# Performance work log

Hardware: AMD Instinct MI355X
Metric: run time of the kernel (lower is better)

## Reference

```python
import jax, jax.numpy as jnp
import numpy as np

EPS = 1e-5  # torch LayerNorm default eps

def _mish(x):
    return x * jnp.tanh(jax.nn.softplus(x))

def _ln(x, g, b):
    mu = jnp.mean(x, axis=-1, keepdims=True)
    var = jnp.mean(jnp.square(x - mu), axis=-1, keepdims=True)
    return (x - mu) * jax.lax.rsqrt(var + EPS) * g + b

def setup_inputs() -> dict:
    key = jax.random.key(0)
    ks = jax.random.split(key, 10)
    B, D, O1, O2, O3 = 65536, 784, 512, 264, 128
    def lin(k, fan_in, shape):
        bound = 1.0 / np.sqrt(fan_in)
        return jax.random.uniform(k, shape, jnp.float32, -bound, bound)
    return {
        "x":  jax.random.uniform(ks[0], (B, D), jnp.float32),
        "W1": lin(ks[1], D,  (O1, D)),   # enFC1, bias=False
        "g1": jnp.ones((O1,), jnp.float32), "b1": jnp.zeros((O1,), jnp.float32),
        "W2": lin(ks[2], O1, (O2, O1)),  # enFC2, bias=False
        "g2": jnp.ones((O2,), jnp.float32), "b2": jnp.zeros((O2,), jnp.float32),
        "W3": lin(ks[3], O2, (O3, O2)),  # enFC3 with bias
        "b3": lin(ks[4], O2, (O3,)),
        "gh": jnp.ones((O3,), jnp.float32), "bh": jnp.zeros((O3,), jnp.float32),
        "D1": lin(ks[5], O3, (O2, O3)),  # deFC1, bias=False
        "g3": jnp.ones((O2,), jnp.float32), "b3n": jnp.zeros((O2,), jnp.float32),
        "D2": lin(ks[6], O2, (O1, O2)),  # deFC2, bias=False
        "g4": jnp.ones((O1,), jnp.float32), "b4": jnp.zeros((O1,), jnp.float32),
        "D3": lin(ks[7], O1, (D, O1)),   # deFC3 with bias
        "bo": lin(ks[8], O1, (D,)),
    }

def reference(x, W1, g1, b1, W2, g2, b2, W3, b3, gh, bh,
              D1, g3, b3n, D2, g4, b4, D3, bo):
    h = _mish(_ln(x @ W1.T, g1, b1))
    h = _mish(_ln(h @ W2.T, g2, b2))
    x_latent = _mish(_ln(h @ W3.T + b3, gh, bh))
    h = _mish(_ln(x_latent @ D1.T, g3, b3n))
    h = _mish(_ln(h @ D2.T, g4, b4))
    out = jax.nn.sigmoid(h @ D3.T + bo)
    return out, jnp.sum(jnp.abs(x_latent))
```

## Files before the change

### kernel.cpp

```cpp
#include <hip/hip_runtime.h>


typedef short bf16x8 __attribute__((ext_vector_type(8)));
typedef float f32x4  __attribute__((ext_vector_type(4)));

#define B_ROWS 65536
#define EPS_LN 1e-5f

static __device__ __forceinline__ unsigned short f2bf(float f) {
    union { float f; unsigned u; } v; v.f = f;
    unsigned r = v.u + 0x7FFFu + ((v.u >> 16) & 1u);
    return (unsigned short)(r >> 16);
}

static __device__ __forceinline__ float mish_f(float x) {
    if (x > 15.f) return x;
    float u = __expf(x);
    float p = __fmaf_rn(u, u, 2.f * u);
    return x * (p / (p + 2.f));
}

static __device__ __forceinline__ void glds16(const void* g, void* l) {
    typedef __attribute__((address_space(3))) unsigned lds_u32;
    typedef __attribute__((address_space(1))) const unsigned glb_u32;
    lds_u32* lp = (lds_u32*)l;
    unsigned lofs = __builtin_amdgcn_readfirstlane((unsigned)(unsigned long long)lp);
    lp = (lds_u32*)(unsigned long long)lofs;
    __builtin_amdgcn_global_load_lds((glb_u32*)g, lp, 16, 0, 0);
}

struct CvtArgs {
    const float* src[6];
    unsigned short* dst[6];
    int O[6], K[6], KP[6];
    int base[7];
};

__global__ void wpad_kernel(CvtArgs a) {
    int b = blockIdx.x;
    int seg = 0;
    while (b >= a.base[seg + 1]) ++seg;
    int r = b - a.base[seg];
    int O = a.O[seg], K = a.K[seg], KP = a.KP[seg];
    const float* s = a.src[seg];
    unsigned short* d = a.dst[seg];
    for (int c = threadIdx.x; c < KP; c += 256) {
        unsigned short v = 0;
        if (r < O && c < K) v = f2bf(s[(size_t)r * K + c]);
        d[(size_t)r * KP + c] = v;
    }
}

template<int KP, int ASTR, int BN, int OREAL, int OSTRIDE, int NKT,
         bool SRCF32, bool HASBIAS, bool ABS, bool LN>
__global__ __launch_bounds__(512, 2)
void layer9(const void* __restrict__ Asrc,
            const unsigned short* __restrict__ Wp,
            const float* __restrict__ gam,
            const float* __restrict__ bet,
            const float* __restrict__ bias,
            void* __restrict__ Aout,
            float* __restrict__ partials)
{
    constexpr int NT   = BN / 64;
    constexpr int NCHW = BN / 8;
    constexpr int NCH  = NCHW + (SRCF32 ? 0 : 16);
    constexpr int MAXC = (NCH + 7) / 8;
    constexpr int ABY  = 128 * 128;
    constexpr int WBY  = BN * 128;

    __shared__ __align__(16) char smem[2 * ABY + 2 * WBY];

    const int tid  = threadIdx.x;
    const int lane = tid & 63;
    const int wu   = __builtin_amdgcn_readfirstlane(tid >> 6);
    const int wr = wu >> 2, wc = wu & 3;
    const int lg = lane >> 4, lc = lane & 15;
    const int row0  = blockIdx.x * 128;
    const int cbase = LN ? 0 : blockIdx.y * BN;

    const int crow = lane >> 3;
    const int sg   = (lane & 7) ^ crow;
    const size_t vofW = ((size_t)crow * KP + (size_t)(sg << 3)) * 2;
    const size_t vofA = ((size_t)crow * ASTR + (size_t)(sg << 3)) * 2;

    auto stage = [&](int t, int b) {
#pragma unroll
        for (int i = 0; i < MAXC; ++i) {
            int c = wu + 8 * i;
            if (c < NCHW) {
                const char* g = (const char*)Wp +
                    ((size_t)(cbase + c * 8) * KP) * 2 + (size_t)t * 128 + vofW;
                glds16(g, smem + (2 * ABY + b * WBY + c * 1024));
            } else if (c < NCH) {
                int ca = c - NCHW;
                const char* g = (const char*)Asrc +
                    ((size_t)(row0 + ca * 8) * ASTR) * 2 + (size_t)t * 128 + vofA;
                glds16(g, smem + (b * ABY + ca * 1024));
            }
        }
    };

    const int ar = tid >> 2, as = tid & 3;
    const float* axp = (const float*)Asrc + (size_t)(row0 + ar) * ASTR + as * 16;
    float4 rA[4];
#pragma unroll
    for (int j = 0; j < 4; ++j) rA[j] = make_float4(0, 0, 0, 0);

    auto loadA1 = [&](int t) {
#pragma unroll
        for (int j = 0; j < 4; ++j) {
            int c0 = t * 64 + as * 16 + j * 4;
            rA[j] = (c0 + 3 < 784) ? *(const float4*)(axp + t * 64 + j * 4)
                                   : make_float4(0, 0, 0, 0);
        }
    };
    auto pubA = [&](int b) {
        union { unsigned short us[8]; uint4 v; } u0, u1;
        u0.us[0] = f2bf(rA[0].x); u0.us[1] = f2bf(rA[0].y);
        u0.us[2] = f2bf(rA[0].z); u0.us[3] = f2bf(rA[0].w);
        u0.us[4] = f2bf(rA[1].x); u0.us[5] = f2bf(rA[1].y);
        u0.us[6] = f2bf(rA[1].z); u0.us[7] = f2bf(rA[1].w);
        u1.us[0] = f2bf(rA[2].x); u1.us[1] = f2bf(rA[2].y);
        u1.us[2] = f2bf(rA[2].z); u1.us[3] = f2bf(rA[2].w);
        u1.us[4] = f2bf(rA[3].x); u1.us[5] = f2bf(rA[3].y);
        u1.us[6] = f2bf(rA[3].z); u1.us[7] = f2bf(rA[3].w);
        int s0 = as * 2, rb = b * ABY + ar * 128, rx = ar & 7;
        *(uint4*)(smem + rb + (((s0    ) ^ rx) << 4)) = u0.v;
        *(uint4*)(smem + rb + (((s0 + 1) ^ rx) << 4)) = u1.v;
    };

    stage(0, 0);
    if constexpr (SRCF32) { loadA1(0); pubA(0); }
    __syncthreads();

    f32x4 acc[4][NT];
#pragma unroll
    for (int a = 0; a < 4; ++a)
#pragma unroll
        for (int c = 0; c < NT; ++c) acc[a][c] = (f32x4){0.f, 0.f, 0.f, 0.f};

    const int f0 = ((lg ^ (lc & 7)) << 4);

    for (int t = 0; t < NKT; ++t) {
        const int bsel = t & 1;
        if (t + 1 < NKT) {
            stage(t + 1, bsel ^ 1);
            if constexpr (SRCF32) loadA1(t + 1);
        }
        const char* Ab = smem + bsel * ABY + (wr * 64 + lc) * 128;
        const char* Bb = smem + 2 * ABY + bsel * WBY + (wc * NT * 16 + lc) * 128;
#pragma unroll
        for (int h = 0; h < 2; ++h) {
            const int fh = f0 ^ (h << 6);
            bf16x8 afr[4], bfr[NT];
#pragma unroll
            for (int a = 0; a < 4; ++a)
                afr[a] = *(const bf16x8*)(Ab + a * 2048 + fh);
#pragma unroll
            for (int c = 0; c < NT; ++c)
                bfr[c] = *(const bf16x8*)(Bb + c * 2048 + fh);
            __builtin_amdgcn_s_setprio(1);
#pragma unroll
            for (int c = 0; c < NT; ++c)
#pragma unroll
                for (int a = 0; a < 4; ++a)
                    acc[a][c] = __builtin_amdgcn_mfma_f32_16x16x32_bf16(afr[a], bfr[c], acc[a][c], 0, 0, 0);
            __builtin_amdgcn_s_setprio(0);
        }
        if constexpr (SRCF32) { if (t + 1 < NKT) pubA(bsel ^ 1); }
        __syncthreads();
    }

    if constexpr (LN) {
        if constexpr (HASBIAS) {
#pragma unroll
            for (int c = 0; c < NT; ++c) {
                int col = wc * NT * 16 + c * 16 + lc;
                float bv = (col < OREAL) ? bias[col] : 0.f;
#pragma unroll
                for (int a = 0; a < 4; ++a)
#pragma unroll
                    for (int r = 0; r < 4; ++r) acc[a][c][r] += bv;
            }
        }
        float ps1[4][4], ps2[4][4];
#pragma unroll
        for (int a = 0; a < 4; ++a)
#pragma unroll
            for (int r = 0; r < 4; ++r) { ps1[a][r] = 0.f; ps2[a][r] = 0.f; }
#pragma unroll
        for (int a = 0; a < 4; ++a)
#pragma unroll
            for (int c = 0; c < NT; ++c)
#pragma unroll
                for (int r = 0; r < 4; ++r) {
                    float v = acc[a][c][r];
                    ps1[a][r] += v;
                    ps2[a][r] = __fmaf_rn(v, v, ps2[a][r]);
                }
#pragma unroll
        for (int m = 1; m < 16; m <<= 1)
#pragma unroll
            for (int a = 0; a < 4; ++a)
#pragma unroll
                for (int r = 0; r < 4; ++r) {
                    ps1[a][r] += __shfl_xor(ps1[a][r], m);
                    ps2[a][r] += __shfl_xor(ps2[a][r], m);
                }

        float* lnP  = (float*)smem;
        float* lnMR = (float*)(smem + 4096);
        float* wsum = (float*)(smem + 5120);

        if (lc == 0) {
#pragma unroll
            for (int a = 0; a < 4; ++a)
#pragma unroll
                for (int r = 0; r < 4; ++r) {
                    int row = wr * 64 + a * 16 + lg * 4 + r;
                    lnP[row * 4 + wc]       = ps1[a][r];
                    lnP[512 + row * 4 + wc] = ps2[a][r];
                }
        }
        __syncthreads();
        if (tid < 128) {
            float s1 = lnP[tid * 4] + lnP[tid * 4 + 1] + lnP[tid * 4 + 2] + lnP[tid * 4 + 3];
            float s2 = lnP[512 + tid * 4] + lnP[512 + tid * 4 + 1] +
                       lnP[512 + tid * 4 + 2] + lnP[512 + tid * 4 + 3];
            float mu = s1 * (1.f / OREAL);
            float var = fmaxf(s2 * (1.f / OREAL) - mu * mu, 0.f);
            lnMR[tid]       = mu;
            lnMR[128 + tid] = rsqrtf(var + EPS_LN);
        }
        __syncthreads();

        float gcol[NT], bcol[NT];
#pragma unroll
        for (int c = 0; c < NT; ++c) {
            int col = wc * NT * 16 + c * 16 + lc;
            gcol[c] = (col < OREAL) ? gam[col] : 0.f;
            bcol[c] = (col < OREAL) ? bet[col] : 0.f;
        }

        float asum = 0.f;
        unsigned short* outp = (unsigned short*)Aout;
#pragma unroll
        for (int a = 0; a < 4; ++a)
#pragma unroll
            for (int r = 0; r < 4; ++r) {
                int rl = wr * 64 + a * 16 + lg * 4 + r;
                float mu = lnMR[rl], rs = lnMR[128 + rl];
                size_t rowoff = (size_t)(row0 + rl) * OSTRIDE;
#pragma unroll
                for (int c = 0; c < NT; ++c) {
                    int col = wc * NT * 16 + c * 16 + lc;
                    if (col < OSTRIDE) {
                        unsigned short outv = 0;
                        if (col < OREAL) {
                            float v = (acc[a][c][r] - mu) * rs * gcol[c] + bcol[c];
                            float mz = mish_f(v);
                            if (ABS) asum += fabsf(mz);
                            outv = f2bf(mz);
                        }
                        outp[rowoff + col] = outv;
                    }
                }
            }

        if constexpr (ABS) {
#pragma unroll
            for (int m = 1; m < 64; m <<= 1) asum += __shfl_xor(asum, m);
            if (lane == 0) wsum[wu] = asum;
            __syncthreads();
            if (tid == 0) {
                float s = 0.f;
                for (int w = 0; w < 8; ++w) s += wsum[w];
                partials[blockIdx.x] = s;
            }
        }
    } else {
        float* outp = (float*)Aout;
#pragma unroll
        for (int c = 0; c < NT; ++c) {
            int col = cbase + wc * NT * 16 + c * 16 + lc;
            bool ok = col < OREAL;
            float bv = ok ? bias[col] : 0.f;
#pragma unroll
            for (int a = 0; a < 4; ++a)
#pragma unroll
                for (int r = 0; r < 4; ++r) {
                    if (ok) {
                        int rl = wr * 64 + a * 16 + lg * 4 + r;
                        float v = acc[a][c][r] + bv;
                        outp[(size_t)(row0 + rl) * OSTRIDE + col] = 1.f / (1.f + __expf(-v));
                    }
                }
        }
    }
}

__global__ __launch_bounds__(512, 2)
void trio(const unsigned short* __restrict__ actP,
          const unsigned short* __restrict__ W2p,
          const unsigned short* __restrict__ W3p,
          const unsigned short* __restrict__ D1p,
          const float* __restrict__ g2, const float* __restrict__ b2,
          const float* __restrict__ gh, const float* __restrict__ bh,
          const float* __restrict__ b3,
          const float* __restrict__ g3, const float* __restrict__ b3n,
          unsigned short* __restrict__ actQ,
          float* __restrict__ partials)
{
    __shared__ __align__(16) char smem[139264];

    const int tid  = threadIdx.x;
    const int lane = tid & 63;
    const int wu   = __builtin_amdgcn_readfirstlane(tid >> 6);
    const int wr = wu >> 2, wc = wu & 3;
    const int lg = lane >> 4, lc = lane & 15;
    const int row0 = blockIdx.x * 128;

    const int sgl = (lane & 3) ^ ((lane >> 3) & 3);
    const size_t vofA  = ((size_t)(lane >> 2) * 512 + (size_t)(sgl << 3)) * 2;
    const size_t vofW2 = vofA;
    const size_t vofW3 = ((size_t)(lane >> 2) * 288 + (size_t)(sgl << 3)) * 2;
    const size_t vofD1 = ((size_t)(lane >> 2) * 128 + (size_t)(sgl << 3)) * 2;

    const int fswz = ((lg ^ ((lc >> 1) & 3)) << 4);

    float* lnP  = (float*)smem;
    float* lnMR = (float*)(smem + 4096);
    float* wsum = (float*)(smem + 5120);

    auto ln_stats = [&](float ps1[4][4], float ps2[4][4], float invO) {
#pragma unroll
        for (int m = 1; m < 16; m <<= 1)
#pragma unroll
            for (int a = 0; a < 4; ++a)
#pragma unroll
                for (int r = 0; r < 4; ++r) {
                    ps1[a][r] += __shfl_xor(ps1[a][r], m);
                    ps2[a][r] += __shfl_xor(ps2[a][r], m);
                }
        if (lc == 0) {
#pragma unroll
            for (int a = 0; a < 4; ++a)
#pragma unroll
                for (int r = 0; r < 4; ++r) {
                    int row = wr * 64 + a * 16 + lg * 4 + r;
                    lnP[row * 4 + wc]       = ps1[a][r];
                    lnP[512 + row * 4 + wc] = ps2[a][r];
                }
        }
        __syncthreads();
        if (tid < 128) {
            float s1 = lnP[tid * 4] + lnP[tid * 4 + 1] + lnP[tid * 4 + 2] + lnP[tid * 4 + 3];
            float s2 = lnP[512 + tid * 4] + lnP[512 + tid * 4 + 1] +
                       lnP[512 + tid * 4 + 2] + lnP[512 + tid * 4 + 3];
            float mu = s1 * invO;
            float var = fmaxf(s2 * invO - mu * mu, 0.f);
            lnMR[tid]       = mu;
            lnMR[128 + tid] = rsqrtf(var + EPS_LN);
        }
        __syncthreads();
    };

    {
        constexpr int NT = 6;
        f32x4 acc[4][NT];
#pragma unroll
        for (int a = 0; a < 4; ++a)
#pragma unroll
            for (int c = 0; c < NT; ++c) acc[a][c] = (f32x4){0.f, 0.f, 0.f, 0.f};

        auto stage1 = [&](int t, int b) {
#pragma unroll
            for (int i = 0; i < 4; ++i) {
                int c = wu + 8 * i;
                if (c < 24) {
                    const char* g = (const char*)W2p +
                        ((size_t)(c * 16) * 512) * 2 + (size_t)t * 64 + vofW2;
                    glds16(g, smem + (16384 + b * 24576 + c * 1024));
                } else {
                    int ca = c - 24;
                    const char* g = (const char*)actP +
                        ((size_t)(row0 + ca * 16) * 512) * 2 + (size_t)t * 64 + vofA;
                    glds16(g, smem + (b * 8192 + ca * 1024));
                }
            }
        };

        stage1(0, 0);
        __syncthreads();
        for (int t = 0; t < 16; ++t) {
            const int bsel = t & 1;
            if (t + 1 < 16) stage1(t + 1, bsel ^ 1);
            const char* Ab = smem + bsel * 8192 + (wr * 64 + lc) * 64 + fswz;
            const char* Bb = smem + 16384 + bsel * 24576 + (wc * 96 + lc) * 64 + fswz;
            bf16x8 afr[4], bfr[NT];
#pragma unroll
            for (int a = 0; a < 4; ++a) afr[a] = *(const bf16x8*)(Ab + a * 1024);
#pragma unroll
            for (int c = 0; c < NT; ++c) bfr[c] = *(const bf16x8*)(Bb + c * 1024);
            __builtin_amdgcn_s_setprio(1);
#pragma unroll
            for (int c = 0; c < NT; ++c)
#pragma unroll
                for (int a = 0; a < 4; ++a)
                    acc[a][c] = __builtin_amdgcn_mfma_f32_16x16x32_bf16(afr[a], bfr[c], acc[a][c], 0, 0, 0);
            __builtin_amdgcn_s_setprio(0);
            __syncthreads();
        }

        float ps1[4][4], ps2[4][4];
#pragma unroll
        for (int a = 0; a < 4; ++a)
#pragma unroll
            for (int r = 0; r < 4; ++r) { ps1[a][r] = 0.f; ps2[a][r] = 0.f; }
#pragma unroll
        for (int a = 0; a < 4; ++a)
#pragma unroll
            for (int c = 0; c < NT; ++c)
#pragma unroll
                for (int r = 0; r < 4; ++r) {
                    float v = acc[a][c][r];
                    ps1[a][r] += v;
                    ps2[a][r] = __fmaf_rn(v, v, ps2[a][r]);
                }
        ln_stats(ps1, ps2, 1.f / 264);

        float gcol[NT], bcol[NT];
#pragma unroll
        for (int c = 0; c < NT; ++c) {
            int col = wc * 96 + c * 16 + lc;
            gcol[c] = (col < 264) ? g2[col] : 0.f;
            bcol[c] = (col < 264) ? b2[col] : 0.f;
        }
#pragma unroll
        for (int a = 0; a < 4; ++a)
#pragma unroll
            for (int r = 0; r < 4; ++r) {
                int rl = wr * 64 + a * 16 + lg * 4 + r;
                float mu = lnMR[rl], rs = lnMR[128 + rl];
                int sx = (rl >> 1) & 3;
                int rowb = 65536 + rl * 576;
#pragma unroll
                for (int c = 0; c < NT; ++c) {
                    int col = wc * 96 + c * 16 + lc;
                    if (col < 288) {
                        unsigned short outv = 0;
                        if (col < 264) {
                            float v = (acc[a][c][r] - mu) * rs * gcol[c] + bcol[c];
                            outv = f2bf(mish_f(v));
                        }
                        int byte = rowb + ((col >> 5) << 6) +
                                   ((((col >> 3) & 3) ^ sx) << 4) + ((col & 7) << 1);
                        *(unsigned short*)(smem + byte) = outv;
                    }
                }
            }
        __syncthreads();
    }

    {
        constexpr int NT = 2;
        f32x4 acc[4][NT];
#pragma unroll
        for (int a = 0; a < 4; ++a)
#pragma unroll
            for (int c = 0; c < NT; ++c) acc[a][c] = (f32x4){0.f, 0.f, 0.f, 0.f};

        auto stage2 = [&](int t, int b) {
            int c = wu;
            const char* g = (const char*)W3p +
                ((size_t)(c * 16) * 288) * 2 + (size_t)t * 64 + vofW3;
            glds16(g, smem + (b * 8192 + c * 1024));
        };

        stage2(0, 0);
        __syncthreads();
        for (int t = 0; t < 9; ++t) {
            const int bsel = t & 1;
            if (t + 1 < 9) stage2(t + 1, bsel ^ 1);
            const char* Ab = smem + 65536 + (wr * 64 + lc) * 576 + t * 64 + fswz;
            const char* Bb = smem + bsel * 8192 + (wc * 32 + lc) * 64 + fswz;
            bf16x8 afr[4], bfr[NT];
#pragma unroll
            for (int a = 0; a < 4; ++a) afr[a] = *(const bf16x8*)(Ab + a * 16 * 576);
#pragma unroll
            for (int c = 0; c < NT; ++c) bfr[c] = *(const bf16x8*)(Bb + c * 1024);
            __builtin_amdgcn_s_setprio(1);
#pragma unroll
            for (int c = 0; c < NT; ++c)
#pragma unroll
                for (int a = 0; a < 4; ++a)
                    acc[a][c] = __builtin_amdgcn_mfma_f32_16x16x32_bf16(afr[a], bfr[c], acc[a][c], 0, 0, 0);
            __builtin_amdgcn_s_setprio(0);
            __syncthreads();
        }

#pragma unroll
        for (int c = 0; c < NT; ++c) {
            int col = wc * 32 + c * 16 + lc;
            float bv = b3[col];
#pragma unroll
            for (int a = 0; a < 4; ++a)
#pragma unroll
                for (int r = 0; r < 4; ++r) acc[a][c][r] += bv;
        }
        float ps1[4][4], ps2[4][4];
#pragma unroll
        for (int a = 0; a < 4; ++a)
#pragma unroll
            for (int r = 0; r < 4; ++r) { ps1[a][r] = 0.f; ps2[a][r] = 0.f; }
#pragma unroll
        for (int a = 0; a < 4; ++a)
#pragma unroll
            for (int c = 0; c < NT; ++c)
#pragma unroll
                for (int r = 0; r < 4; ++r) {
                    float v = acc[a][c][r];
                    ps1[a][r] += v;
                    ps2[a][r] = __fmaf_rn(v, v, ps2[a][r]);
                }
        ln_stats(ps1, ps2, 1.f / 128);

        float gcol[NT], bcol[NT];
#pragma unroll
        for (int c = 0; c < NT; ++c) {
            int col = wc * 32 + c * 16 + lc;
            gcol[c] = gh[col];
            bcol[c] = bh[col];
        }
        float asum = 0.f;
#pragma unroll
        for (int a = 0; a < 4; ++a)
#pragma unroll
            for (int r = 0; r < 4; ++r) {
                int rl = wr * 64 + a * 16 + lg * 4 + r;
                float mu = lnMR[rl], rs = lnMR[128 + rl];
                int sx = (rl >> 1) & 3;
                int rowb = 16384 + rl * 256;
#pragma unroll
                for (int c = 0; c < NT; ++c) {
                    int col = wc * 32 + c * 16 + lc;
                    float v = (acc[a][c][r] - mu) * rs * gcol[c] + bcol[c];
                    float mz = mish_f(v);
                    asum += fabsf(mz);
                    int byte = rowb + ((col >> 5) << 6) +
                               ((((col >> 3) & 3) ^ sx) << 4) + ((col & 7) << 1);
                    *(unsigned short*)(smem + byte) = f2bf(mz);
                }
            }
#pragma unroll
        for (int m = 1; m < 64; m <<= 1) asum += __shfl_xor(asum, m);
        if (lane == 0) wsum[wu] = asum;
        __syncthreads();
        if (tid == 0) {
            float s = 0.f;
            for (int w = 0; w < 8; ++w) s += wsum[w];
            partials[blockIdx.x] = s;
        }
        __syncthreads();
    }

    {
        constexpr int NT = 6;
        f32x4 acc[4][NT];
#pragma unroll
        for (int a = 0; a < 4; ++a)
#pragma unroll
            for (int c = 0; c < NT; ++c) acc[a][c] = (f32x4){0.f, 0.f, 0.f, 0.f};

        auto stage3 = [&](int t, int b) {
#pragma unroll
            for (int i = 0; i < 3; ++i) {
                int c = wu + 8 * i;
                const char* g = (const char*)D1p +
                    ((size_t)(c * 16) * 128) * 2 + (size_t)t * 64 + vofD1;
                glds16(g, smem + (65536 + b * 24576 + c * 1024));
            }
        };

        stage3(0, 0);
        __syncthreads();
        for (int t = 0; t < 4; ++t) {
            const int bsel = t & 1;
            if (t + 1 < 4) stage3(t + 1, bsel ^ 1);
            const char* Ab = smem + 16384 + (wr * 64 + lc) * 256 + t * 64 + fswz;
            const char* Bb = smem + 65536 + bsel * 24576 + (wc * 96 + lc) * 64 + fswz;
            bf16x8 afr[4], bfr[NT];
#pragma unroll
            for (int a = 0; a < 4; ++a) afr[a] = *(const bf16x8*)(Ab + a * 16 * 256);
#pragma unroll
            for (int c = 0; c < NT; ++c) bfr[c] = *(const bf16x8*)(Bb + c * 1024);
            __builtin_amdgcn_s_setprio(1);
#pragma unroll
            for (int c = 0; c < NT; ++c)
#pragma unroll
                for (int a = 0; a < 4; ++a)
                    acc[a][c] = __builtin_amdgcn_mfma_f32_16x16x32_bf16(afr[a], bfr[c], acc[a][c], 0, 0, 0);
            __builtin_amdgcn_s_setprio(0);
            __syncthreads();
        }

        float ps1[4][4], ps2[4][4];
#pragma unroll
        for (int a = 0; a < 4; ++a)
#pragma unroll
            for (int r = 0; r < 4; ++r) { ps1[a][r] = 0.f; ps2[a][r] = 0.f; }
#pragma unroll
        for (int a = 0; a < 4; ++a)
#pragma unroll
            for (int c = 0; c < NT; ++c)
#pragma unroll
                for (int r = 0; r < 4; ++r) {
                    float v = acc[a][c][r];
                    ps1[a][r] += v;
                    ps2[a][r] = __fmaf_rn(v, v, ps2[a][r]);
                }
        ln_stats(ps1, ps2, 1.f / 264);

        float gcol[NT], bcol[NT];
#pragma unroll
        for (int c = 0; c < NT; ++c) {
            int col = wc * 96 + c * 16 + lc;
            gcol[c] = (col < 264) ? g3[col] : 0.f;
            bcol[c] = (col < 264) ? b3n[col] : 0.f;
        }
#pragma unroll
        for (int a = 0; a < 4; ++a)
#pragma unroll
            for (int r = 0; r < 4; ++r) {
                int rl = wr * 64 + a * 16 + lg * 4 + r;
                float mu = lnMR[rl], rs = lnMR[128 + rl];
                size_t rowoff = (size_t)(row0 + rl) * 320;
#pragma unroll
                for (int c = 0; c < NT; ++c) {
                    int col = wc * 96 + c * 16 + lc;
                    if (col < 320) {
                        unsigned short outv = 0;
                        if (col < 264) {
                            float v = (acc[a][c][r] - mu) * rs * gcol[c] + bcol[c];
                            outv = f2bf(mish_f(v));
                        }
                        actQ[rowoff + col] = outv;
                    }
                }
            }
    }
}

__global__ void reduce_abs(const float* __restrict__ partials, float* __restrict__ out) {
    __shared__ float sm[256];
    float s = 0.f;
    for (int i = threadIdx.x; i < 512; i += 256) s += partials[i];
    sm[threadIdx.x] = s;
    __syncthreads();
    for (int step = 128; step > 0; step >>= 1) {
        if (threadIdx.x < step) sm[threadIdx.x] += sm[threadIdx.x + step];
        __syncthreads();
    }
    if (threadIdx.x == 0) out[0] = sm[0];
}

extern "C" void kernel_launch(void* const* d_in, const int* in_sizes, int n_in,
                              void* d_out, int out_size, void* d_ws, size_t ws_size,
                              hipStream_t stream)
{
    const float* x   = (const float*)d_in[0];
    const float* W1  = (const float*)d_in[1];
    const float* g1  = (const float*)d_in[2];
    const float* b1  = (const float*)d_in[3];
    const float* W2  = (const float*)d_in[4];
    const float* g2  = (const float*)d_in[5];
    const float* b2  = (const float*)d_in[6];
    const float* W3  = (const float*)d_in[7];
    const float* b3  = (const float*)d_in[8];
    const float* gh  = (const float*)d_in[9];
    const float* bh  = (const float*)d_in[10];
    const float* D1  = (const float*)d_in[11];
    const float* g3  = (const float*)d_in[12];
    const float* b3n = (const float*)d_in[13];
    const float* D2  = (const float*)d_in[14];
    const float* g4  = (const float*)d_in[15];
    const float* b4  = (const float*)d_in[16];
    const float* D3  = (const float*)d_in[17];
    const float* bo  = (const float*)d_in[18];

    char* ws = (char*)d_ws;
    size_t off = 0;
    auto alloc = [&](size_t bytes) -> char* {
        char* p = ws + off;
        off += (bytes + 255) & ~(size_t)255;
        return p;
    };
    unsigned short* W1p = (unsigned short*)alloc((size_t)512 * 832 * 2);
    unsigned short* W2p = (unsigned short*)alloc((size_t)384 * 512 * 2);
    unsigned short* W3p = (unsigned short*)alloc((size_t)128 * 288 * 2);
    unsigned short* D1p = (unsigned short*)alloc((size_t)384 * 128 * 2);
    unsigned short* D2p = (unsigned short*)alloc((size_t)512 * 320 * 2);
    unsigned short* D3p = (unsigned short*)alloc((size_t)896 * 512 * 2);
    unsigned short* actP = (unsigned short*)alloc((size_t)B_ROWS * 512 * 2);
    unsigned short* actQ = (unsigned short*)alloc((size_t)B_ROWS * 320 * 2);
    float* partials = (float*)alloc(512 * 4);

    CvtArgs ca;
    ca.src[0] = W1; ca.dst[0] = W1p; ca.O[0] = 512; ca.K[0] = 784; ca.KP[0] = 832;
    ca.src[1] = W2; ca.dst[1] = W2p; ca.O[1] = 264; ca.K[1] = 512; ca.KP[1] = 512;
    ca.src[2] = W3; ca.dst[2] = W3p; ca.O[2] = 128; ca.K[2] = 264; ca.KP[2] = 288;
    ca.src[3] = D1; ca.dst[3] = D1p; ca.O[3] = 264; ca.K[3] = 128; ca.KP[3] = 128;
    ca.src[4] = D2; ca.dst[4] = D2p; ca.O[4] = 512; ca.K[4] = 264; ca.KP[4] = 320;
    ca.src[5] = D3; ca.dst[5] = D3p; ca.O[5] = 784; ca.K[5] = 512; ca.KP[5] = 512;
    ca.base[0] = 0;    ca.base[1] = 512;  ca.base[2] = 896;
    ca.base[3] = 1024; ca.base[4] = 1408; ca.base[5] = 1920; ca.base[6] = 2816;
    wpad_kernel<<<2816, 256, 0, stream>>>(ca);

    const int NB = B_ROWS / 128;

    layer9<832, 784, 512, 512, 512, 13, true,  false, false, true>
        <<<NB, 512, 0, stream>>>(x, W1p, g1, b1, nullptr, actP, nullptr);
    trio<<<NB, 512, 0, stream>>>(actP, W2p, W3p, D1p,
                                 g2, b2, gh, bh, b3, g3, b3n, actQ, partials);
    layer9<320, 320, 512, 512, 512, 5,  false, false, false, true>
        <<<NB, 512, 0, stream>>>(actQ, D2p, g4, b4, nullptr, actP, nullptr);
    dim3 g6(NB, 2);
    layer9<512, 512, 448, 784, 784, 8,  false, true,  false, false>
        <<<g6, 512, 0, stream>>>(actP, D3p, nullptr, nullptr, bo, d_out, nullptr);

    reduce_abs<<<1, 256, 0, stream>>>(partials, (float*)d_out + (size_t)B_ROWS * 784);
}
```

Measured before the change: 421.8 us.

## Fuse decoder layer two into trio kernel and widen output GEMM tile

The decoder D2 GEMM with its LayerNorm and Mish moves into the existing fused kernel, which now becomes a four-layer kernel. The 264-wide latent-decoder activation stays in shared memory instead of being written to and re-read from global memory, and one kernel launch is removed. A new output kernel computes all 784 output columns per 128-row block instead of splitting them across two blocks, so each activation tile is read once. The costs are shared memory near the per-CU limit, a single-buffered, synchronised weight load loop in the new D2 stage, and a large accumulator (14 tiles per wave) that may push register pressure and occupancy.

```diff
diff --git a/kernel.cpp b/kernel.cpp
--- a/kernel.cpp
+++ b/kernel.cpp
@@ -300,19 +300,27 @@
     }
 }
 
+#define H2_OFF  65536
+#define H3_OFF  122880
+#define H4_OFF  49152
+#define W5_OFF  122880
+#define LN_OFF  155648
+
 __global__ __launch_bounds__(512, 2)
-void trio(const unsigned short* __restrict__ actP,
+void quad(const unsigned short* __restrict__ actP,
           const unsigned short* __restrict__ W2p,
           const unsigned short* __restrict__ W3p,
           const unsigned short* __restrict__ D1p,
+          const unsigned short* __restrict__ D2p,
           const float* __restrict__ g2, const float* __restrict__ b2,
           const float* __restrict__ gh, const float* __restrict__ bh,
           const float* __restrict__ b3,
           const float* __restrict__ g3, const float* __restrict__ b3n,
-          unsigned short* __restrict__ actQ,
+          const float* __restrict__ g4, const float* __restrict__ b4,
+          unsigned short* __restrict__ actH,
           float* __restrict__ partials)
 {
-    __shared__ __align__(16) char smem[139264];
+    __shared__ __align__(16) char smem[160800];
 
     const int tid  = threadIdx.x;
     const int lane = tid & 63;
@@ -326,12 +334,13 @@
     const size_t vofW2 = vofA;
     const size_t vofW3 = ((size_t)(lane >> 2) * 288 + (size_t)(sgl << 3)) * 2;
     const size_t vofD1 = ((size_t)(lane >> 2) * 128 + (size_t)(sgl << 3)) * 2;
+    const size_t vofW5 = ((size_t)(lane >> 2) * 320 + (size_t)(sgl << 3)) * 2;
 
     const int fswz = ((lg ^ ((lc >> 1) & 3)) << 4);
 
-    float* lnP  = (float*)smem;
-    float* lnMR = (float*)(smem + 4096);
-    float* wsum = (float*)(smem + 5120);
+    float* lnP  = (float*)(smem + LN_OFF);
+    float* lnMR = (float*)(smem + LN_OFF + 4096);
+    float* wsum = (float*)(smem + LN_OFF + 5120);
 
     auto ln_stats = [&](float ps1[4][4], float ps2[4][4], float invO) {
 #pragma unroll
@@ -444,7 +453,7 @@
                 int rl = wr * 64 + a * 16 + lg * 4 + r;
                 float mu = lnMR[rl], rs = lnMR[128 + rl];
                 int sx = (rl >> 1) & 3;
-                int rowb = 65536 + rl * 576;
+                int rowb = H2_OFF + rl * 576;
 #pragma unroll
                 for (int c = 0; c < NT; ++c) {
                     int col = wc * 96 + c * 16 + lc;
@@ -483,7 +492,7 @@
         for (int t = 0; t < 9; ++t) {
             const int bsel = t & 1;
             if (t + 1 < 9) stage2(t + 1, bsel ^ 1);
-            const char* Ab = smem + 65536 + (wr * 64 + lc) * 576 + t * 64 + fswz;
+            const char* Ab = smem + H2_OFF + (wr * 64 + lc) * 576 + t * 64 + fswz;
             const char* Bb = smem + bsel * 8192 + (wc * 32 + lc) * 64 + fswz;
             bf16x8 afr[4], bfr[NT];
 #pragma unroll
@@ -541,7 +550,7 @@
                 int rl = wr * 64 + a * 16 + lg * 4 + r;
                 float mu = lnMR[rl], rs = lnMR[128 + rl];
                 int sx = (rl >> 1) & 3;
-                int rowb = 16384 + rl * 256;
+                int rowb = H3_OFF + rl * 256;
 #pragma unroll
                 for (int c = 0; c < NT; ++c) {
                     int col = wc * 32 + c * 16 + lc;
@@ -579,7 +588,7 @@
                 int c = wu + 8 * i;
                 const char* g = (const char*)D1p +
                     ((size_t)(c * 16) * 128) * 2 + (size_t)t * 64 + vofD1;
-                glds16(g, smem + (65536 + b * 24576 + c * 1024));
+                glds16(g, smem + (b * 24576 + c * 1024));
             }
         };
 
@@ -588,8 +597,8 @@
         for (int t = 0; t < 4; ++t) {
             const int bsel = t & 1;
             if (t + 1 < 4) stage3(t + 1, bsel ^ 1);
-            const char* Ab = smem + 16384 + (wr * 64 + lc) * 256 + t * 64 + fswz;
-            const char* Bb = smem + 65536 + bsel * 24576 + (wc * 96 + lc) * 64 + fswz;
+            const char* Ab = smem + H3_OFF + (wr * 64 + lc) * 256 + t * 64 + fswz;
+            const char* Bb = smem + bsel * 24576 + (wc * 96 + lc) * 64 + fswz;
             bf16x8 afr[4], bfr[NT];
 #pragma unroll
             for (int a = 0; a < 4; ++a) afr[a] = *(const bf16x8*)(Ab + a * 16 * 256);
@@ -635,18 +644,186 @@
             for (int r = 0; r < 4; ++r) {
                 int rl = wr * 64 + a * 16 + lg * 4 + r;
                 float mu = lnMR[rl], rs = lnMR[128 + rl];
-                size_t rowoff = (size_t)(row0 + rl) * 320;
+                int sx = (rl >> 1) & 3;
+                int rowb = H4_OFF + rl * 576;
 #pragma unroll
                 for (int c = 0; c < NT; ++c) {
                     int col = wc * 96 + c * 16 + lc;
-                    if (col < 320) {
+                    if (col < 288) {
                         unsigned short outv = 0;
                         if (col < 264) {
                             float v = (acc[a][c][r] - mu) * rs * gcol[c] + bcol[c];
                             outv = f2bf(mish_f(v));
                         }
-                        actQ[rowoff + col] = outv;
+                        int byte = rowb + ((col >> 5) << 6) +
+                                   ((((col >> 3) & 3) ^ sx) << 4) + ((col & 7) << 1);
+                        *(unsigned short*)(smem + byte) = outv;
                     }
+                }
+            }
+        __syncthreads();
+    }
+
+    {
+        constexpr int NT = 8;
+        f32x4 acc[4][NT];
+#pragma unroll
+        for (int a = 0; a < 4; ++a)
+#pragma unroll
+            for (int c = 0; c < NT; ++c) acc[a][c] = (f32x4){0.f, 0.f, 0.f, 0.f};
+
+        auto stage4 = [&](int t) {
+#pragma unroll
+            for (int i = 0; i < 4; ++i) {
+                int c = wu + 8 * i;
+                const char* g = (const char*)D2p +
+                    ((size_t)(c * 16) * 320) * 2 + (size_t)t * 64 + vofW5;
+                glds16(g, smem + (W5_OFF + c * 1024));
+            }
+        };
+
+        for (int t = 0; t < 9; ++t) {
+            stage4(t);
+            __syncthreads();
+            const char* Ab = smem + H4_OFF + (wr * 64 + lc) * 576 + t * 64 + fswz;
+            const char* Bb = smem + W5_OFF + (wc * 128 + lc) * 64 + fswz;
+            bf16x8 afr[4], bfr[NT];
+#pragma unroll
+            for (int a = 0; a < 4; ++a) afr[a] = *(const bf16x8*)(Ab + a * 16 * 576);
+#pragma unroll
+            for (int c = 0; c < NT; ++c) bfr[c] = *(const bf16x8*)(Bb + c * 1024);
+            __builtin_amdgcn_s_setprio(1);
+#pragma unroll
+            for (int c = 0; c < NT; ++c)
+#pragma unroll
+                for (int a = 0; a < 4; ++a)
+                    acc[a][c] = __builtin_amdgcn_mfma_f32_16x16x32_bf16(afr[a], bfr[c], acc[a][c], 0, 0, 0);
+            __builtin_amdgcn_s_setprio(0);
+            __syncthreads();
+        }
+
+        float ps1[4][4], ps2[4][4];
+#pragma unroll
+        for (int a = 0; a < 4; ++a)
+#pragma unroll
+            for (int r = 0; r < 4; ++r) { ps1[a][r] = 0.f; ps2[a][r] = 0.f; }
+#pragma unroll
+        for (int a = 0; a < 4; ++a)
+#pragma unroll
+            for (int c = 0; c < NT; ++c)
+#pragma unroll
+                for (int r = 0; r < 4; ++r) {
+                    float v = acc[a][c][r];
+                    ps1[a][r] += v;
+                    ps2[a][r] = __fmaf_rn(v, v, ps2[a][r]);
+                }
+        ln_stats(ps1, ps2, 1.f / 512);
+
+        float gcol[NT], bcol[NT];
+#pragma unroll
+        for (int c = 0; c < NT; ++c) {
+            int col = wc * 128 + c * 16 + lc;
+            gcol[c] = g4[col];
+            bcol[c] = b4[col];
+        }
+#pragma unroll
+        for (int a = 0; a < 4; ++a)
+#pragma unroll
+            for (int r = 0; r < 4; ++r) {
+                int rl = wr * 64 + a * 16 + lg * 4 + r;
+                float mu = lnMR[rl], rs = lnMR[128 + rl];
+                size_t rowoff = (size_t)(row0 + rl) * 512;
+#pragma unroll
+                for (int c = 0; c < NT; ++c) {
+                    int col = wc * 128 + c * 16 + lc;
+                    float v = (acc[a][c][r] - mu) * rs * gcol[c] + bcol[c];
+                    actH[rowoff + col] = f2bf(mish_f(v));
+                }
+            }
+    }
+}
+
+__global__ __launch_bounds__(512, 2)
+void layer_out(const unsigned short* __restrict__ actH,
+               const unsigned short* __restrict__ D3p,
+               const float* __restrict__ bo,
+               float* __restrict__ Out)
+{
+    constexpr int NT = 14, NCHW = 56, NCH = 64, MAXC = 8;
+    constexpr int ABY = 8192, WBY = 57344;
+    __shared__ __align__(16) char smem[2 * ABY + 2 * WBY];
+
+    const int tid  = threadIdx.x;
+    const int lane = tid & 63;
+    const int wu   = __builtin_amdgcn_readfirstlane(tid >> 6);
+    const int wr = wu >> 2, wc = wu & 3;
+    const int lg = lane >> 4, lc = lane & 15;
+    const int row0 = blockIdx.x * 128;
+
+    const int sgl = (lane & 3) ^ ((lane >> 3) & 3);
+    const size_t vof = ((size_t)(lane >> 2) * 512 + (size_t)(sgl << 3)) * 2;
+
+    auto stage = [&](int t, int b) {
+#pragma unroll
+        for (int i = 0; i < MAXC; ++i) {
+            int c = wu + 8 * i;
+            if (c < NCHW) {
+                const char* g = (const char*)D3p +
+                    ((size_t)(c * 16) * 512) * 2 + (size_t)t * 64 + vof;
+                glds16(g, smem + (2 * ABY + b * WBY + c * 1024));
+            } else {
+                int ca = c - NCHW;
+                const char* g = (const char*)actH +
+                    ((size_t)(row0 + ca * 16) * 512) * 2 + (size_t)t * 64 + vof;
+                glds16(g, smem + (b * ABY + ca * 1024));
+            }
+        }
+    };
+
+    stage(0, 0);
+    __syncthreads();
+
+    f32x4 acc[4][NT];
+#pragma unroll
+    for (int a = 0; a < 4; ++a)
+#pragma unroll
+        for (int c = 0; c < NT; ++c) acc[a][c] = (f32x4){0.f, 0.f, 0.f, 0.f};
+
+    const int fswz = ((lg ^ ((lc >> 1) & 3)) << 4);
+
+    for (int t = 0; t < 16; ++t) {
+        const int bsel = t & 1;
+        if (t + 1 < 16) stage(t + 1, bsel ^ 1);
+        const char* Ab = smem + bsel * ABY + (wr * 64 + lc) * 64 + fswz;
+        const char* Bb = smem + 2 * ABY + bsel * WBY + (wc * 224 + lc) * 64 + fswz;
+        bf16x8 afr[4], bfr[NT];
+#pragma unroll
+        for (int a = 0; a < 4; ++a) afr[a] = *(const bf16x8*)(Ab + a * 1024);
+#pragma unroll
+        for (int c = 0; c < NT; ++c) bfr[c] = *(const bf16x8*)(Bb + c * 1024);
+        __builtin_amdgcn_s_setprio(1);
+#pragma unroll
+        for (int c = 0; c < NT; ++c)
+#pragma unroll
+            for (int a = 0; a < 4; ++a)
+                acc[a][c] = __builtin_amdgcn_mfma_f32_16x16x32_bf16(afr[a], bfr[c], acc[a][c], 0, 0, 0);
+        __builtin_amdgcn_s_setprio(0);
+        __syncthreads();
+    }
+
+#pragma unroll
+    for (int c = 0; c < NT; ++c) {
+        int col = wc * 224 + c * 16 + lc;
+        bool ok = col < 784;
+        float bv = ok ? bo[col] : 0.f;
+#pragma unroll
+        for (int a = 0; a < 4; ++a)
+#pragma unroll
+            for (int r = 0; r < 4; ++r) {
+                if (ok) {
+                    int rl = wr * 64 + a * 16 + lg * 4 + r;
+                    float v = acc[a][c][r] + bv;
+                    Out[(size_t)(row0 + rl) * 784 + col] = 1.f / (1.f + __expf(-v));
                 }
             }
     }
@@ -703,7 +880,7 @@
     unsigned short* D2p = (unsigned short*)alloc((size_t)512 * 320 * 2);
     unsigned short* D3p = (unsigned short*)alloc((size_t)896 * 512 * 2);
     unsigned short* actP = (unsigned short*)alloc((size_t)B_ROWS * 512 * 2);
-    unsigned short* actQ = (unsigned short*)alloc((size_t)B_ROWS * 320 * 2);
+    unsigned short* actH = (unsigned short*)alloc((size_t)B_ROWS * 512 * 2);
     float* partials = (float*)alloc(512 * 4);
 
     CvtArgs ca;
@@ -721,13 +898,10 @@
 
     layer9<832, 784, 512, 512, 512, 13, true,  false, false, true>
         <<<NB, 512, 0, stream>>>(x, W1p, g1, b1, nullptr, actP, nullptr);
-    trio<<<NB, 512, 0, stream>>>(actP, W2p, W3p, D1p,
-                                 g2, b2, gh, bh, b3, g3, b3n, actQ, partials);
-    layer9<320, 320, 512, 512, 512, 5,  false, false, false, true>
-        <<<NB, 512, 0, stream>>>(actQ, D2p, g4, b4, nullptr, actP, nullptr);
-    dim3 g6(NB, 2);
-    layer9<512, 512, 448, 784, 784, 8,  false, true,  false, false>
-        <<<g6, 512, 0, stream>>>(actP, D3p, nullptr, nullptr, bo, d_out, nullptr);
+    quad<<<NB, 512, 0, stream>>>(actP, W2p, W3p, D1p, D2p,
+                                 g2, b2, gh, bh, b3, g3, b3n, g4, b4,
+                                 actH, partials);
+    layer_out<<<NB, 512, 0, stream>>>(actH, D3p, bo, (float*)d_out);
 
     reduce_abs<<<1, 256, 0, stream>>>(partials, (float*)d_out + (size_t)B_ROWS * 784);
 }
```

Result: slower. 648.5 us (+53.8%).
